# Optimization experiments

Measured on AMD Instinct MI355X. Metric: run time of the kernel, lower is better.

Reference implementation:

```python
import jax, jax.numpy as jnp
import numpy as np


def setup_inputs() -> dict:
    key = jax.random.key(0)
    ks = jax.random.split(key, 6)
    b, t, e = 8, 2048, 1024
    q = jax.random.normal(ks[0], (b, t, e), dtype=jnp.float32)
    k = jax.random.normal(ks[1], (b, t, e), dtype=jnp.float32)
    v = jax.random.normal(ks[2], (b, t, e), dtype=jnp.float32)
    # nn.Linear(emb, emb, bias=False) weights, stored as [out, in] like torch
    s = 1.0 / np.sqrt(e)
    Wq = jax.random.uniform(ks[3], (e, e), dtype=jnp.float32, minval=-s, maxval=s)
    Wk = jax.random.uniform(ks[4], (e, e), dtype=jnp.float32, minval=-s, maxval=s)
    Wv = jax.random.uniform(ks[5], (e, e), dtype=jnp.float32, minval=-s, maxval=s)
    return {"q": q, "k": k, "v": v, "Wq": Wq, "Wk": Wk, "Wv": Wv}


def reference(q, k, v, Wq, Wk, Wv):
    b, t_q, e = q.shape
    t_k = k.shape[1]
    scale = e ** 0.25  # each of Q and K divided by e^(1/4) -> combined 1/sqrt(e)
    queries = jnp.einsum('bte,fe->btf', q, Wq) / scale
    keys = jnp.einsum('bte,fe->btf', k, Wk) / scale
    values = jnp.einsum('bte,fe->btf', v, Wv)
    dot = jnp.einsum('bqe,bke->bqk', queries, keys)  # [b, t_q, t_k]
    # self.mask=True: mask_(dot, -inf, mask_diagonal=False) zeroes strictly-upper triangle
    causal = jnp.triu(jnp.ones((t_q, t_k), dtype=bool), k=1)  # True above diagonal
    dot = jnp.where(causal[None, :, :], -jnp.inf, dot)
    attn = jax.nn.softmax(dot, axis=2)
    out = jnp.einsum('bqk,bke->bqe', attn, values)
    return out
```

## Files before the change

### kernel.cpp

```cpp
#include <hip/hip_runtime.h>
#include <hip/hip_bf16.h>


typedef short short8 __attribute__((ext_vector_type(8)));
typedef float f32x4 __attribute__((ext_vector_type(4)));
typedef int   int4v __attribute__((ext_vector_type(4)));

static constexpr int B_ = 8;
static constexpr int T_ = 2048;
static constexpr int E_ = 1024;

__device__ __forceinline__ float bf2f(ushort u) {
    union { unsigned int i; float f; } x; x.i = ((unsigned int)u) << 16; return x.f;
}
__device__ __forceinline__ ushort f2bf(float f) {
    union { float f; unsigned int i; } x; x.f = f;
    unsigned int r = x.i + 0x7fffu + ((x.i >> 16) & 1u);
    return (ushort)(r >> 16);
}
__device__ __forceinline__ short8 cvt8(f32x4 a, f32x4 b) {
    short8 r;
    union { __hip_bfloat162 h; unsigned int u; } p;
    unsigned int* ru = (unsigned int*)&r;
    p.h = __float22bfloat162_rn(make_float2(a[0], a[1])); ru[0] = p.u;
    p.h = __float22bfloat162_rn(make_float2(a[2], a[3])); ru[1] = p.u;
    p.h = __float22bfloat162_rn(make_float2(b[0], b[1])); ru[2] = p.u;
    p.h = __float22bfloat162_rn(make_float2(b[2], b[3])); ru[3] = p.u;
    return r;
}

__device__ __forceinline__ void async16(const ushort* g, ushort* l) {
    __builtin_amdgcn_global_load_lds(
        (const __attribute__((address_space(1))) unsigned int*)g,
        (__attribute__((address_space(3))) unsigned int*)l, 16, 0, 0);
}
__device__ __forceinline__ void async16f(const float* g, float* l) {
    __builtin_amdgcn_global_load_lds(
        (const __attribute__((address_space(1))) unsigned int*)g,
        (__attribute__((address_space(3))) unsigned int*)l, 16, 0, 0);
}

__device__ __forceinline__ void gemm_tile64(const ushort* __restrict__ A, int lda,
                                            const ushort* __restrict__ Bm, int ldb,
                                            int ksteps, f32x4 (&acc)[4][4],
                                            ushort* As, ushort* Bs)
{
    const int tid = threadIdx.x, lane = tid & 63, wave = tid >> 6;
    const int wr = (wave >> 1) * 64, wc = (wave & 1) * 64;
    const int srow = lane >> 3;
    const int scol = ((lane & 7) ^ srow) * 8;
    const int frow = lane & 15, q4 = lane >> 4;

    for (int ks = 0; ks < ksteps; ++ks) {
        const int k0 = ks * 64;
        __syncthreads();
#pragma unroll
        for (int j = 0; j < 4; ++j) {
            const int c = wave * 4 + j;
            const int grow = c * 8 + srow;
            async16(A  + (size_t)grow * lda + k0 + scol, As + c * 512);
            async16(Bm + (size_t)grow * ldb + k0 + scol, Bs + c * 512);
        }
        __syncthreads();

        short8 af[4][2], bf[4][2];
#pragma unroll
        for (int i = 0; i < 4; ++i) {
            const int ra = wr + i * 16 + frow;
            const int rb = wc + i * 16 + frow;
            const int sw = frow & 7;
#pragma unroll
            for (int kk = 0; kk < 2; ++kk) {
                const int g = (kk * 4 + q4) ^ sw;
                af[i][kk] = *(const short8*)(As + ra * 64 + g * 8);
                bf[i][kk] = *(const short8*)(Bs + rb * 64 + g * 8);
            }
        }
#pragma unroll
        for (int kk = 0; kk < 2; ++kk)
#pragma unroll
            for (int mi = 0; mi < 4; ++mi)
#pragma unroll
                for (int ni = 0; ni < 4; ++ni)
                    acc[mi][ni] = __builtin_amdgcn_mfma_f32_16x16x32_bf16(
                        af[mi][kk], bf[ni][kk], acc[mi][ni], 0, 0, 0);
    }
}

__global__ __launch_bounds__(256)
void cvtW_kernel(const float* __restrict__ w0, const float* __restrict__ w1,
                 const float* __restrict__ w2, ushort* __restrict__ d)
{
    const float* s = blockIdx.y == 0 ? w0 : (blockIdx.y == 1 ? w1 : w2);
    ushort* dd = d + (size_t)blockIdx.y * E_ * E_;
    const int idx = (blockIdx.x * 256 + threadIdx.x) * 8;
    f32x4 a = *(const f32x4*)(s + idx);
    f32x4 b = *(const f32x4*)(s + idx + 4);
    *(short8*)(dd + idx) = cvt8(a, b);
}

__global__ __launch_bounds__(256, 2)
void proj_kernel(const float* __restrict__ q, const float* __restrict__ k,
                 const float* __restrict__ v, const ushort* __restrict__ Wb,
                 ushort* __restrict__ Q, ushort* __restrict__ Kp,
                 ushort* __restrict__ Vt)
{
    __shared__ float  Asf[128 * 32];
    __shared__ ushort Bs[128 * 32];
    const int z = blockIdx.z;
    const float* A = (z == 0 ? q : (z == 1 ? k : v)) + (size_t)blockIdx.x * 128 * E_;
    const ushort* W = Wb + (size_t)z * E_ * E_ + (size_t)blockIdx.y * 128 * E_;

    const int tid = threadIdx.x, lane = tid & 63, wave = tid >> 6;
    const int wr = (wave >> 1) * 64, wc = (wave & 1) * 64;
    const int sArow = lane >> 3;
    const int sAcol = ((lane & 7) ^ sArow) * 4;
    const int sBrow = lane >> 2;
    const int sBcol = ((lane & 3) ^ ((lane >> 3) & 3)) * 8;
    const int frow = lane & 15, q4 = lane >> 4;

    f32x4 acc[4][4];
#pragma unroll
    for (int i = 0; i < 4; ++i)
#pragma unroll
        for (int j = 0; j < 4; ++j) acc[i][j] = (f32x4){0.f, 0.f, 0.f, 0.f};

    for (int ks = 0; ks < E_ / 32; ++ks) {
        const int k0 = ks * 32;
        __syncthreads();
#pragma unroll
        for (int j = 0; j < 4; ++j) {
            const int c = wave * 4 + j;
            async16f(A + (size_t)(c * 8 + sArow) * E_ + k0 + sAcol, Asf + c * 256);
        }
#pragma unroll
        for (int j = 0; j < 2; ++j) {
            const int c = wave * 2 + j;
            async16(W + (size_t)(c * 16 + sBrow) * E_ + k0 + sBcol, Bs + c * 512);
        }
        __syncthreads();

        short8 af[4], bf[4];
#pragma unroll
        for (int i = 0; i < 4; ++i) {
            const int R = wr + i * 16 + frow;
            const int g0 = (q4 * 2) ^ (frow & 7);
            const int g1 = g0 ^ 1;
            f32x4 lo = *(const f32x4*)(Asf + R * 32 + g0 * 4);
            f32x4 hi = *(const f32x4*)(Asf + R * 32 + g1 * 4);
            af[i] = cvt8(lo, hi);
        }
#pragma unroll
        for (int i = 0; i < 4; ++i) {
            const int R = wc + i * 16 + frow;
            const int g = q4 ^ ((frow >> 1) & 3);
            bf[i] = *(const short8*)(Bs + R * 32 + g * 8);
        }
#pragma unroll
        for (int mi = 0; mi < 4; ++mi)
#pragma unroll
            for (int ni = 0; ni < 4; ++ni)
                acc[mi][ni] = __builtin_amdgcn_mfma_f32_16x16x32_bf16(
                    af[mi], bf[ni], acc[mi][ni], 0, 0, 0);
    }

    const float scale = (z == 2) ? 1.0f : 0.17677669529663687f;
    if (z < 2) {
        ushort* D = (z == 0 ? Q : Kp);
#pragma unroll
        for (int mi = 0; mi < 4; ++mi)
#pragma unroll
            for (int r = 0; r < 4; ++r) {
                const int row = blockIdx.x * 128 + wr + mi * 16 + (lane >> 4) * 4 + r;
#pragma unroll
                for (int ni = 0; ni < 4; ++ni) {
                    const int col = blockIdx.y * 128 + wc + ni * 16 + (lane & 15);
                    D[(size_t)row * E_ + col] = f2bf(acc[mi][ni][r] * scale);
                }
            }
    } else {
#pragma unroll
        for (int mi = 0; mi < 4; ++mi)
#pragma unroll
            for (int r = 0; r < 4; ++r) {
                const int rowg = blockIdx.x * 128 + wr + mi * 16 + (lane >> 4) * 4 + r;
                const int bb = rowg >> 11, tl = rowg & 2047;
#pragma unroll
                for (int ni = 0; ni < 4; ++ni) {
                    const int col = blockIdx.y * 128 + wc + ni * 16 + (lane & 15);
                    Vt[(size_t)bb * E_ * T_ + (size_t)col * T_ + tl] = f2bf(acc[mi][ni][r]);
                }
            }
    }
}

__global__ __launch_bounds__(256, 2)
void score_kernel(const ushort* __restrict__ Q, const ushort* __restrict__ K,
                  ushort* __restrict__ S)
{
    __shared__ ushort As[128 * 64];
    __shared__ ushort Bs[128 * 64];
    const int t = blockIdx.x, b = blockIdx.y;
    int br = (int)((sqrtf(8.0f * t + 1.0f) - 1.0f) * 0.5f);
    while ((br + 1) * (br + 2) / 2 <= t) ++br;
    while (br * (br + 1) / 2 > t) --br;
    const int bc = t - br * (br + 1) / 2;

    const ushort* A  = Q + ((size_t)b * T_ + br * 128) * E_;
    const ushort* Bm = K + ((size_t)b * T_ + bc * 128) * E_;

    f32x4 acc[4][4];
#pragma unroll
    for (int i = 0; i < 4; ++i)
#pragma unroll
        for (int j = 0; j < 4; ++j) acc[i][j] = (f32x4){0.f, 0.f, 0.f, 0.f};

    gemm_tile64(A, E_, Bm, E_, E_ / 64, acc, As, Bs);

    const int lane = threadIdx.x & 63, wave = threadIdx.x >> 6;
    const int wr = (wave >> 1) * 64, wc = (wave & 1) * 64;
    ushort* Sb = S + (size_t)b * T_ * T_;
#pragma unroll
    for (int mi = 0; mi < 4; ++mi)
#pragma unroll
        for (int r = 0; r < 4; ++r) {
            const int row = br * 128 + wr + mi * 16 + (lane >> 4) * 4 + r;
#pragma unroll
            for (int ni = 0; ni < 4; ++ni) {
                const int col = bc * 128 + wc + ni * 16 + (lane & 15);
                float val = acc[mi][ni][r];
                if (col > row) val = -1e30f;
                Sb[(size_t)row * T_ + col] = f2bf(val);
            }
        }
}

__global__ __launch_bounds__(256)
void softmax_kernel(ushort* __restrict__ S)
{
    const int gr = blockIdx.x;
    const int b = gr >> 11, i = gr & 2047;
    ushort* row = S + (size_t)b * T_ * T_ + (size_t)i * T_;
    const int Lpad = ((i >> 7) + 1) * 128;
    const int tid = threadIdx.x, lane = tid & 63, wave = tid >> 6;
    __shared__ float red[4];

    const int j0 = tid * 8;
    const bool act = j0 < Lpad;
    float xv[8];
    if (act) {
        int4v dv = *(const int4v*)(row + j0);
        const ushort* u = (const ushort*)&dv;
#pragma unroll
        for (int t = 0; t < 8; ++t) xv[t] = bf2f(u[t]);
    }

    float m = -1e30f;
    if (act)
#pragma unroll
        for (int t = 0; t < 8; ++t) m = fmaxf(m, xv[t]);
#pragma unroll
    for (int o = 32; o; o >>= 1) m = fmaxf(m, __shfl_xor(m, o, 64));
    if (lane == 0) red[wave] = m;
    __syncthreads();
    m = fmaxf(fmaxf(red[0], red[1]), fmaxf(red[2], red[3]));
    __syncthreads();

    float s = 0.f;
    if (act)
#pragma unroll
        for (int t = 0; t < 8; ++t) { xv[t] = __expf(xv[t] - m); s += xv[t]; }
#pragma unroll
    for (int o = 32; o; o >>= 1) s += __shfl_xor(s, o, 64);
    if (lane == 0) red[wave] = s;
    __syncthreads();
    s = red[0] + red[1] + red[2] + red[3];
    const float inv = 1.0f / s;

    if (act) {
        int4v dv;
        ushort* u = (ushort*)&dv;
#pragma unroll
        for (int t = 0; t < 8; ++t) u[t] = f2bf(xv[t] * inv);
        *(int4v*)(row + j0) = dv;
    }
}

__global__ __launch_bounds__(256, 2)
void out_kernel(const ushort* __restrict__ P, const ushort* __restrict__ Vt,
                float* __restrict__ O)
{
    __shared__ ushort As[128 * 64];
    __shared__ ushort Bs[128 * 64];
    const int bc = blockIdx.x, br = blockIdx.y, b = blockIdx.z;
    const ushort* A  = P  + (size_t)b * T_ * T_ + (size_t)(br * 128) * T_;
    const ushort* Bm = Vt + (size_t)b * E_ * T_ + (size_t)(bc * 128) * T_;
    const int ksteps = (br + 1) * 2;

    f32x4 acc[4][4];
#pragma unroll
    for (int i = 0; i < 4; ++i)
#pragma unroll
        for (int j = 0; j < 4; ++j) acc[i][j] = (f32x4){0.f, 0.f, 0.f, 0.f};

    gemm_tile64(A, T_, Bm, T_, ksteps, acc, As, Bs);

    const int lane = threadIdx.x & 63, wave = threadIdx.x >> 6;
    const int wr = (wave >> 1) * 64, wc = (wave & 1) * 64;
    float* Ob = O + (size_t)b * T_ * E_;
#pragma unroll
    for (int mi = 0; mi < 4; ++mi)
#pragma unroll
        for (int r = 0; r < 4; ++r) {
            const int row = br * 128 + wr + mi * 16 + (lane >> 4) * 4 + r;
#pragma unroll
            for (int ni = 0; ni < 4; ++ni) {
                const int col = bc * 128 + wc + ni * 16 + (lane & 15);
                Ob[(size_t)row * E_ + col] = acc[mi][ni][r];
            }
        }
}

extern "C" void kernel_launch(void* const* d_in, const int* in_sizes, int n_in,
                              void* d_out, int out_size, void* d_ws, size_t ws_size,
                              hipStream_t stream)
{
    const float* q  = (const float*)d_in[0];
    const float* k  = (const float*)d_in[1];
    const float* v  = (const float*)d_in[2];
    const float* Wq = (const float*)d_in[3];
    const float* Wk = (const float*)d_in[4];
    const float* Wv = (const float*)d_in[5];
    float* out = (float*)d_out;

    const size_t nQKV = (size_t)B_ * T_ * E_;
    const size_t nW   = (size_t)E_ * E_;
    ushort* Q  = (ushort*)d_ws;
    ushort* K  = Q + nQKV;
    ushort* Vt = K + nQKV;
    ushort* S  = Vt + nQKV;
    ushort* Wb = S;

    cvtW_kernel<<<dim3(nW / 2048, 3), 256, 0, stream>>>(Wq, Wk, Wv, Wb);
    proj_kernel<<<dim3(128, 8, 3), 256, 0, stream>>>(q, k, v, Wb, Q, K, Vt);
    score_kernel<<<dim3(136, B_), 256, 0, stream>>>(Q, K, S);
    softmax_kernel<<<dim3(B_ * T_), 256, 0, stream>>>(S);
    out_kernel<<<dim3(E_ / 128, T_ / 128, B_), 256, 0, stream>>>(S, Vt, out);
}
```

Before: 506.0 us.

## Double projection K-tile to 64 and schedule longest causal out tiles first

Result: no change. 509.0 us (+0.6%).

```diff
diff --git a/kernel.cpp b/kernel.cpp
--- a/kernel.cpp
+++ b/kernel.cpp
@@ -105,18 +105,16 @@
                  ushort* __restrict__ Q, ushort* __restrict__ Kp,
                  ushort* __restrict__ Vt)
 {
-    __shared__ float  Asf[128 * 32];
-    __shared__ ushort Bs[128 * 32];
+    __shared__ float  Asf[128 * 64];
+    __shared__ ushort Bs[128 * 64];
     const int z = blockIdx.z;
     const float* A = (z == 0 ? q : (z == 1 ? k : v)) + (size_t)blockIdx.x * 128 * E_;
     const ushort* W = Wb + (size_t)z * E_ * E_ + (size_t)blockIdx.y * 128 * E_;
 
     const int tid = threadIdx.x, lane = tid & 63, wave = tid >> 6;
     const int wr = (wave >> 1) * 64, wc = (wave & 1) * 64;
-    const int sArow = lane >> 3;
-    const int sAcol = ((lane & 7) ^ sArow) * 4;
-    const int sBrow = lane >> 2;
-    const int sBcol = ((lane & 3) ^ ((lane >> 3) & 3)) * 8;
+    const int aRowIn = lane >> 4;
+    const int bRowIn = lane >> 3;
     const int frow = lane & 15, q4 = lane >> 4;
 
     f32x4 acc[4][4];
@@ -125,43 +123,48 @@
 #pragma unroll
         for (int j = 0; j < 4; ++j) acc[i][j] = (f32x4){0.f, 0.f, 0.f, 0.f};
 
-    for (int ks = 0; ks < E_ / 32; ++ks) {
-        const int k0 = ks * 32;
+    for (int ks = 0; ks < E_ / 64; ++ks) {
+        const int k0 = ks * 64;
         __syncthreads();
+#pragma unroll
+        for (int j = 0; j < 8; ++j) {
+            const int c = wave * 8 + j;
+            const int row = c * 4 + aRowIn;
+            const int sg = (lane & 15) ^ (row & 7);
+            async16f(A + (size_t)row * E_ + k0 + sg * 4, Asf + c * 256);
+        }
 #pragma unroll
         for (int j = 0; j < 4; ++j) {
             const int c = wave * 4 + j;
-            async16f(A + (size_t)(c * 8 + sArow) * E_ + k0 + sAcol, Asf + c * 256);
-        }
-#pragma unroll
-        for (int j = 0; j < 2; ++j) {
-            const int c = wave * 2 + j;
-            async16(W + (size_t)(c * 16 + sBrow) * E_ + k0 + sBcol, Bs + c * 512);
+            const int row = c * 8 + bRowIn;
+            const int sg = (lane & 7) ^ (row & 7);
+            async16(W + (size_t)row * E_ + k0 + sg * 8, Bs + c * 512);
         }
         __syncthreads();
 
-        short8 af[4], bf[4];
-#pragma unroll
-        for (int i = 0; i < 4; ++i) {
-            const int R = wr + i * 16 + frow;
-            const int g0 = (q4 * 2) ^ (frow & 7);
-            const int g1 = g0 ^ 1;
-            f32x4 lo = *(const f32x4*)(Asf + R * 32 + g0 * 4);
-            f32x4 hi = *(const f32x4*)(Asf + R * 32 + g1 * 4);
-            af[i] = cvt8(lo, hi);
-        }
-#pragma unroll
-        for (int i = 0; i < 4; ++i) {
-            const int R = wc + i * 16 + frow;
-            const int g = q4 ^ ((frow >> 1) & 3);
-            bf[i] = *(const short8*)(Bs + R * 32 + g * 8);
-        }
-#pragma unroll
-        for (int mi = 0; mi < 4; ++mi)
-#pragma unroll
-            for (int ni = 0; ni < 4; ++ni)
-                acc[mi][ni] = __builtin_amdgcn_mfma_f32_16x16x32_bf16(
-                    af[mi], bf[ni], acc[mi][ni], 0, 0, 0);
+#pragma unroll
+        for (int kk = 0; kk < 2; ++kk) {
+            short8 af[4], bf[4];
+#pragma unroll
+            for (int i = 0; i < 4; ++i) {
+                const int Ra = wr + i * 16 + frow;
+                const int sw = frow & 7;
+                const int g0 = (kk * 8 + q4 * 2) ^ sw;
+                const int g1 = g0 ^ 1;
+                f32x4 lo = *(const f32x4*)(Asf + Ra * 64 + g0 * 4);
+                f32x4 hi = *(const f32x4*)(Asf + Ra * 64 + g1 * 4);
+                af[i] = cvt8(lo, hi);
+                const int Rb = wc + i * 16 + frow;
+                const int gb = (kk * 4 + q4) ^ sw;
+                bf[i] = *(const short8*)(Bs + Rb * 64 + gb * 8);
+            }
+#pragma unroll
+            for (int mi = 0; mi < 4; ++mi)
+#pragma unroll
+                for (int ni = 0; ni < 4; ++ni)
+                    acc[mi][ni] = __builtin_amdgcn_mfma_f32_16x16x32_bf16(
+                        af[mi], bf[ni], acc[mi][ni], 0, 0, 0);
+        }
     }
 
     const float scale = (z == 2) ? 1.0f : 0.17677669529663687f;
@@ -292,7 +295,8 @@
 {
     __shared__ ushort As[128 * 64];
     __shared__ ushort Bs[128 * 64];
-    const int bc = blockIdx.x, br = blockIdx.y, b = blockIdx.z;
+    const int bc = blockIdx.x, b = blockIdx.z;
+    const int br = (int)gridDim.y - 1 - (int)blockIdx.y;
     const ushort* A  = P  + (size_t)b * T_ * T_ + (size_t)(br * 128) * T_;
     const ushort* Bm = Vt + (size_t)b * E_ * T_ + (size_t)(bc * 128) * T_;
     const int ksteps = (br + 1) * 2;
```

## Double-buffer LDS tiles in GEMM kernels and remap block order for locality

Applied to the files above, without the earlier changes.

After: 570.0 us. 1.13x slower.

```diff
diff --git a/kernel.cpp b/kernel.cpp
--- a/kernel.cpp
+++ b/kernel.cpp
@@ -40,10 +40,10 @@
         (__attribute__((address_space(3))) unsigned int*)l, 16, 0, 0);
 }
 
-__device__ __forceinline__ void gemm_tile64(const ushort* __restrict__ A, int lda,
-                                            const ushort* __restrict__ Bm, int ldb,
-                                            int ksteps, f32x4 (&acc)[4][4],
-                                            ushort* As, ushort* Bs)
+__device__ __forceinline__ void gemm_tile64_db(const ushort* __restrict__ A, int lda,
+                                               const ushort* __restrict__ Bm, int ldb,
+                                               int ksteps, f32x4 (&acc)[4][4],
+                                               ushort* As, ushort* Bs)
 {
     const int tid = threadIdx.x, lane = tid & 63, wave = tid >> 6;
     const int wr = (wave >> 1) * 64, wc = (wave & 1) * 64;
@@ -51,18 +51,30 @@
     const int scol = ((lane & 7) ^ srow) * 8;
     const int frow = lane & 15, q4 = lane >> 4;
 
+#pragma unroll
+    for (int j = 0; j < 4; ++j) {
+        const int c = wave * 4 + j;
+        const int grow = c * 8 + srow;
+        async16(A  + (size_t)grow * lda + scol, As + c * 512);
+        async16(Bm + (size_t)grow * ldb + scol, Bs + c * 512);
+    }
+    __syncthreads();
+
+    int cur = 0;
     for (int ks = 0; ks < ksteps; ++ks) {
-        const int k0 = ks * 64;
-        __syncthreads();
-#pragma unroll
-        for (int j = 0; j < 4; ++j) {
-            const int c = wave * 4 + j;
-            const int grow = c * 8 + srow;
-            async16(A  + (size_t)grow * lda + k0 + scol, As + c * 512);
-            async16(Bm + (size_t)grow * ldb + k0 + scol, Bs + c * 512);
-        }
-        __syncthreads();
-
+        if (ks + 1 < ksteps) {
+            const int k0 = (ks + 1) * 64;
+            const int nb = (cur ^ 1) * 8192;
+#pragma unroll
+            for (int j = 0; j < 4; ++j) {
+                const int c = wave * 4 + j;
+                const int grow = c * 8 + srow;
+                async16(A  + (size_t)grow * lda + k0 + scol, As + nb + c * 512);
+                async16(Bm + (size_t)grow * ldb + k0 + scol, Bs + nb + c * 512);
+            }
+        }
+        const ushort* Ab = As + cur * 8192;
+        const ushort* Bb = Bs + cur * 8192;
         short8 af[4][2], bf[4][2];
 #pragma unroll
         for (int i = 0; i < 4; ++i) {
@@ -72,8 +84,8 @@
 #pragma unroll
             for (int kk = 0; kk < 2; ++kk) {
                 const int g = (kk * 4 + q4) ^ sw;
-                af[i][kk] = *(const short8*)(As + ra * 64 + g * 8);
-                bf[i][kk] = *(const short8*)(Bs + rb * 64 + g * 8);
+                af[i][kk] = *(const short8*)(Ab + ra * 64 + g * 8);
+                bf[i][kk] = *(const short8*)(Bb + rb * 64 + g * 8);
             }
         }
 #pragma unroll
@@ -84,6 +96,8 @@
                 for (int ni = 0; ni < 4; ++ni)
                     acc[mi][ni] = __builtin_amdgcn_mfma_f32_16x16x32_bf16(
                         af[mi][kk], bf[ni][kk], acc[mi][ni], 0, 0, 0);
+        __syncthreads();
+        cur ^= 1;
     }
 }
 
@@ -105,11 +119,18 @@
                  ushort* __restrict__ Q, ushort* __restrict__ Kp,
                  ushort* __restrict__ Vt)
 {
-    __shared__ float  Asf[128 * 32];
-    __shared__ ushort Bs[128 * 32];
-    const int z = blockIdx.z;
-    const float* A = (z == 0 ? q : (z == 1 ? k : v)) + (size_t)blockIdx.x * 128 * E_;
-    const ushort* W = Wb + (size_t)z * E_ * E_ + (size_t)blockIdx.y * 128 * E_;
+    __shared__ float  Asf[2 * 128 * 32];
+    __shared__ ushort Bs[2 * 128 * 32];
+
+    const int bid = blockIdx.x;
+    const int n   = (bid & 7) * 384 + (bid >> 3);
+    const int z   = n >> 10;
+    const int rem = n & 1023;
+    const int by  = rem & 7;
+    const int bx  = rem >> 3;
+
+    const float* A = (z == 0 ? q : (z == 1 ? k : v)) + (size_t)bx * 128 * E_;
+    const ushort* W = Wb + (size_t)z * E_ * E_ + (size_t)by * 128 * E_;
 
     const int tid = threadIdx.x, lane = tid & 63, wave = tid >> 6;
     const int wr = (wave >> 1) * 64, wc = (wave & 1) * 64;
@@ -125,36 +146,54 @@
 #pragma unroll
         for (int j = 0; j < 4; ++j) acc[i][j] = (f32x4){0.f, 0.f, 0.f, 0.f};
 
-    for (int ks = 0; ks < E_ / 32; ++ks) {
-        const int k0 = ks * 32;
-        __syncthreads();
-#pragma unroll
-        for (int j = 0; j < 4; ++j) {
-            const int c = wave * 4 + j;
-            async16f(A + (size_t)(c * 8 + sArow) * E_ + k0 + sAcol, Asf + c * 256);
-        }
-#pragma unroll
-        for (int j = 0; j < 2; ++j) {
-            const int c = wave * 2 + j;
-            async16(W + (size_t)(c * 16 + sBrow) * E_ + k0 + sBcol, Bs + c * 512);
-        }
-        __syncthreads();
-
+#pragma unroll
+    for (int j = 0; j < 4; ++j) {
+        const int c = wave * 4 + j;
+        async16f(A + (size_t)(c * 8 + sArow) * E_ + sAcol, Asf + c * 256);
+    }
+#pragma unroll
+    for (int j = 0; j < 2; ++j) {
+        const int c = wave * 2 + j;
+        async16(W + (size_t)(c * 16 + sBrow) * E_ + sBcol, Bs + c * 512);
+    }
+    __syncthreads();
+
+    int cur = 0;
+    const int nt = E_ / 32;
+    for (int ks = 0; ks < nt; ++ks) {
+        if (ks + 1 < nt) {
+            const int k0 = (ks + 1) * 32;
+            const int na = (cur ^ 1) * 4096, nb = (cur ^ 1) * 4096;
+#pragma unroll
+            for (int j = 0; j < 4; ++j) {
+                const int c = wave * 4 + j;
+                async16f(A + (size_t)(c * 8 + sArow) * E_ + k0 + sAcol,
+                         Asf + na + c * 256);
+            }
+#pragma unroll
+            for (int j = 0; j < 2; ++j) {
+                const int c = wave * 2 + j;
+                async16(W + (size_t)(c * 16 + sBrow) * E_ + k0 + sBcol,
+                        Bs + nb + c * 512);
+            }
+        }
+        const float*  Ab = Asf + cur * 4096;
+        const ushort* Bb = Bs  + cur * 4096;
         short8 af[4], bf[4];
 #pragma unroll
         for (int i = 0; i < 4; ++i) {
             const int R = wr + i * 16 + frow;
             const int g0 = (q4 * 2) ^ (frow & 7);
             const int g1 = g0 ^ 1;
-            f32x4 lo = *(const f32x4*)(Asf + R * 32 + g0 * 4);
-            f32x4 hi = *(const f32x4*)(Asf + R * 32 + g1 * 4);
+            f32x4 lo = *(const f32x4*)(Ab + R * 32 + g0 * 4);
+            f32x4 hi = *(const f32x4*)(Ab + R * 32 + g1 * 4);
             af[i] = cvt8(lo, hi);
         }
 #pragma unroll
         for (int i = 0; i < 4; ++i) {
             const int R = wc + i * 16 + frow;
             const int g = q4 ^ ((frow >> 1) & 3);
-            bf[i] = *(const short8*)(Bs + R * 32 + g * 8);
+            bf[i] = *(const short8*)(Bb + R * 32 + g * 8);
         }
 #pragma unroll
         for (int mi = 0; mi < 4; ++mi)
@@ -162,6 +201,8 @@
             for (int ni = 0; ni < 4; ++ni)
                 acc[mi][ni] = __builtin_amdgcn_mfma_f32_16x16x32_bf16(
                     af[mi], bf[ni], acc[mi][ni], 0, 0, 0);
+        __syncthreads();
+        cur ^= 1;
     }
 
     const float scale = (z == 2) ? 1.0f : 0.17677669529663687f;
@@ -171,10 +212,10 @@
         for (int mi = 0; mi < 4; ++mi)
 #pragma unroll
             for (int r = 0; r < 4; ++r) {
-                const int row = blockIdx.x * 128 + wr + mi * 16 + (lane >> 4) * 4 + r;
+                const int row = bx * 128 + wr + mi * 16 + (lane >> 4) * 4 + r;
 #pragma unroll
                 for (int ni = 0; ni < 4; ++ni) {
-                    const int col = blockIdx.y * 128 + wc + ni * 16 + (lane & 15);
+                    const int col = by * 128 + wc + ni * 16 + (lane & 15);
                     D[(size_t)row * E_ + col] = f2bf(acc[mi][ni][r] * scale);
                 }
             }
@@ -183,11 +224,11 @@
         for (int mi = 0; mi < 4; ++mi)
 #pragma unroll
             for (int r = 0; r < 4; ++r) {
-                const int rowg = blockIdx.x * 128 + wr + mi * 16 + (lane >> 4) * 4 + r;
+                const int rowg = bx * 128 + wr + mi * 16 + (lane >> 4) * 4 + r;
                 const int bb = rowg >> 11, tl = rowg & 2047;
 #pragma unroll
                 for (int ni = 0; ni < 4; ++ni) {
-                    const int col = blockIdx.y * 128 + wc + ni * 16 + (lane & 15);
+                    const int col = by * 128 + wc + ni * 16 + (lane & 15);
                     Vt[(size_t)bb * E_ * T_ + (size_t)col * T_ + tl] = f2bf(acc[mi][ni][r]);
                 }
             }
@@ -198,9 +239,10 @@
 void score_kernel(const ushort* __restrict__ Q, const ushort* __restrict__ K,
                   ushort* __restrict__ S)
 {
-    __shared__ ushort As[128 * 64];
-    __shared__ ushort Bs[128 * 64];
-    const int t = blockIdx.x, b = blockIdx.y;
+    __shared__ ushort As[2 * 128 * 64];
+    __shared__ ushort Bs[2 * 128 * 64];
+    const int b = blockIdx.y;
+    const int t = (blockIdx.x & 7) * 17 + (blockIdx.x >> 3);
     int br = (int)((sqrtf(8.0f * t + 1.0f) - 1.0f) * 0.5f);
     while ((br + 1) * (br + 2) / 2 <= t) ++br;
     while (br * (br + 1) / 2 > t) --br;
@@ -215,7 +257,7 @@
 #pragma unroll
         for (int j = 0; j < 4; ++j) acc[i][j] = (f32x4){0.f, 0.f, 0.f, 0.f};
 
-    gemm_tile64(A, E_, Bm, E_, E_ / 64, acc, As, Bs);
+    gemm_tile64_db(A, E_, Bm, E_, E_ / 64, acc, As, Bs);
 
     const int lane = threadIdx.x & 63, wave = threadIdx.x >> 6;
     const int wr = (wave >> 1) * 64, wc = (wave & 1) * 64;
@@ -290,9 +332,10 @@
 void out_kernel(const ushort* __restrict__ P, const ushort* __restrict__ Vt,
                 float* __restrict__ O)
 {
-    __shared__ ushort As[128 * 64];
-    __shared__ ushort Bs[128 * 64];
-    const int bc = blockIdx.x, br = blockIdx.y, b = blockIdx.z;
+    __shared__ ushort As[2 * 128 * 64];
+    __shared__ ushort Bs[2 * 128 * 64];
+    const int bc = blockIdx.x, b = blockIdx.z;
+    const int br = (int)gridDim.y - 1 - (int)blockIdx.y;
     const ushort* A  = P  + (size_t)b * T_ * T_ + (size_t)(br * 128) * T_;
     const ushort* Bm = Vt + (size_t)b * E_ * T_ + (size_t)(bc * 128) * T_;
     const int ksteps = (br + 1) * 2;
@@ -303,7 +346,7 @@
 #pragma unroll
         for (int j = 0; j < 4; ++j) acc[i][j] = (f32x4){0.f, 0.f, 0.f, 0.f};
 
-    gemm_tile64(A, T_, Bm, T_, ksteps, acc, As, Bs);
+    gemm_tile64_db(A, T_, Bm, T_, ksteps, acc, As, Bs);
 
     const int lane = threadIdx.x & 63, wave = threadIdx.x >> 6;
     const int wr = (wave >> 1) * 64, wc = (wave & 1) * 64;
@@ -342,7 +385,7 @@
     ushort* Wb = S;
 
     cvtW_kernel<<<dim3(nW / 2048, 3), 256, 0, stream>>>(Wq, Wk, Wv, Wb);
-    proj_kernel<<<dim3(128, 8, 3), 256, 0, stream>>>(q, k, v, Wb, Q, K, Vt);
+    proj_kernel<<<dim3(3072), 256, 0, stream>>>(q, k, v, Wb, Q, K, Vt);
     score_kernel<<<dim3(136, B_), 256, 0, stream>>>(Q, K, S);
     softmax_kernel<<<dim3(B_ * T_), 256, 0, stream>>>(S);
     out_kernel<<<dim3(E_ / 128, T_ / 128, B_), 256, 0, stream>>>(S, Vt, out);
```
